# Kernel optimization log

Measured on AMD Instinct MI355X. Metric: run time of the kernel, lower is better.

## Reference

```python
import jax, jax.numpy as jnp
import numpy as np
from jax import lax

B, T, F = 8, 512, 128          # batch, mel time, mel freq
DM, DS, DC, EXP, NL = 384, 16, 4, 2, 12
DI = EXP * DM                   # 768 inner width
DTR = (DM + 15) // 16           # 24, mamba_ssm dt_rank='auto'
PT = PF = 16
L = (T // PT) * (F // PF)       # 256 patches
NC = 4


def setup_inputs() -> dict:
    key = jax.random.key(0)
    ks = iter(jax.random.split(key, 24))
    def n(shape, s=0.02):
        return jax.random.normal(next(ks), shape, jnp.float32) * s
    return {
        "x": jax.random.normal(next(ks), (B, T, F), jnp.float32),
        "patch_w": n((DM, PT, PF)),
        "patch_b": jnp.zeros((DM,), jnp.float32),
        "pos_embed": n((1, L, DM)),
        "ln_g": jnp.ones((NL, DM), jnp.float32),
        "ln_b": jnp.zeros((NL, DM), jnp.float32),
        "in_proj_w": n((NL, 2 * DI, DM)),
        "conv_w": n((NL, DI, DC), 0.1),
        "conv_b": jnp.zeros((NL, DI), jnp.float32),
        "x_proj_w": n((NL, DTR + 2 * DS, DI)),
        "dt_proj_w": n((NL, DI, DTR), 0.1),
        "dt_proj_b": n((NL, DI), 0.1),
        "A_log": jnp.tile(jnp.log(jnp.arange(1, DS + 1, dtype=jnp.float32))[None, None, :], (NL, DI, 1)),
        "Dskip": jnp.ones((NL, DI), jnp.float32),
        "out_proj_w": n((NL, DM, DI)),
        "fn_g": jnp.ones((DM,), jnp.float32),
        "fn_b": jnp.zeros((DM,), jnp.float32),
        "head_w": n((NC, DM)),
        "head_b": jnp.zeros((NC,), jnp.float32),
    }


def _layernorm(x, g, b):
    m = x.mean(-1, keepdims=True)
    v = jnp.var(x, axis=-1, keepdims=True)
    return (x - m) * lax.rsqrt(v + 1e-5) * g + b


def _silu(v):
    return v * jax.nn.sigmoid(v)


def _mamba_block(x, p):
    # x: [B, L, DM]; residual Mamba block (pre-LN, dropout=identity in eval)
    ln_g, ln_b, Wi, cw, cb, Wx, Wdt, bdt, A_log, Dsk, Wo = p
    res = x
    h = _layernorm(x, ln_g, ln_b)
    xz = jnp.einsum('bld,ed->ble', h, Wi)          # [B,L,2*DI]
    u, z = jnp.split(xz, 2, axis=-1)
    # causal depthwise conv1d, kernel DC (small, unrolled)
    up = jnp.pad(u, ((0, 0), (DC - 1, 0), (0, 0)))
    u = sum(up[:, k:k + L, :] * cw[:, k] for k in range(DC)) + cb
    u = _silu(u)
    proj = jnp.einsum('bld,ed->ble', u, Wx)        # [B,L,DTR+2*DS]
    dt, Bm, Cm = jnp.split(proj, [DTR, DTR + DS], axis=-1)
    delta = jax.nn.softplus(jnp.einsum('blr,dr->bld', dt, Wdt) + bdt)  # [B,L,DI]
    A = -jnp.exp(A_log)                            # [DI, DS]
    dA = jnp.exp(delta[..., None] * A)             # [B,L,DI,DS]
    dBu = (delta * u)[..., None] * Bm[:, :, None, :]

    def step(hst, inp):
        dA_t, dBu_t, C_t = inp
        hst = dA_t * hst + dBu_t                   # [B,DI,DS]
        return hst, jnp.einsum('bdn,bn->bd', hst, C_t)

    h0 = jnp.zeros((x.shape[0], DI, DS), x.dtype)
    _, ys = lax.scan(step, h0, (dA.swapaxes(0, 1), dBu.swapaxes(0, 1), Cm.swapaxes(0, 1)))
    y = ys.swapaxes(0, 1) + u * Dsk                # [B,L,DI]
    y = y * _silu(z)
    return res + jnp.einsum('bld,ed->ble', y, Wo)


def reference(x, patch_w, patch_b, pos_embed, ln_g, ln_b, in_proj_w, conv_w, conv_b,
              x_proj_w, dt_proj_w, dt_proj_b, A_log, Dskip, out_proj_w,
              fn_g, fn_b, head_w, head_b):
    Bn = x.shape[0]
    # patch embed = non-overlapping 16x16 conv == blocked reshape + einsum
    patches = x.reshape(Bn, T // PT, PT, F // PF, PF)
    tok = jnp.einsum('bhpwq,dpq->bhwd', patches, patch_w) + patch_b
    tok = tok.reshape(Bn, L, DM) + pos_embed

    def layer(carry, p):
        return _mamba_block(carry, p), None

    tok, _ = lax.scan(layer, tok, (ln_g, ln_b, in_proj_w, conv_w, conv_b,
                                   x_proj_w, dt_proj_w, dt_proj_b, A_log, Dskip, out_proj_w))
    tok = _layernorm(tok, fn_g, fn_b)
    pooled = tok.mean(axis=1)
    return pooled @ head_w.T + head_b
```

## Files before the change

### kernel.cpp

```cpp
#include <hip/hip_runtime.h>
#include <math.h>

namespace {

constexpr int kB   = 8;
constexpr int kL   = 256;
constexpr int kTok = 2048;
constexpr int kDM  = 384;
constexpr int kDI  = 768;
constexpr int kDS  = 16;
constexpr int kDTR = 24;
constexpr int kPROJ = 56;
constexpr int kNL  = 12;

constexpr int kWIN  = 2 * kDI * kDM;
constexpr int kWOUT = kDM * kDI;
constexpr int kWX   = kPROJ * kDI;
constexpr int kWTOT = kWIN + kWOUT + kWX;

typedef float f32x4 __attribute__((ext_vector_type(4)));
typedef short short8 __attribute__((ext_vector_type(8)));

__device__ __forceinline__ float softplus_f(float x) {
  return (x > 20.f) ? x : log1pf(__expf(x));
}
__device__ __forceinline__ float silu_f(float x) {
  return x / (1.f + __expf(-x));
}
__device__ __forceinline__ unsigned short f2bf(float f) {
  union { float f; unsigned u; } v; v.f = f;
  unsigned r = v.u + 0x7FFFu + ((v.u >> 16) & 1u);
  return (unsigned short)(r >> 16);
}
__device__ __forceinline__ float bf2f(unsigned short u) {
  return __uint_as_float((unsigned)u << 16);
}

__global__ __launch_bounds__(256) void patch_gemm_k(
    const float* __restrict__ x, const float* __restrict__ Bw,
    const float* __restrict__ bias, const float* __restrict__ pos,
    float* __restrict__ C) {
  __shared__ float As[16][68];
  __shared__ float Bs[16][68];
  int tid = threadIdx.x;
  int bm = blockIdx.y * 64;
  int bn = blockIdx.x * 64;
  int lr = tid >> 2;
  int lk = (tid & 3) << 2;
  int tm = (tid >> 4) << 2;
  int tn = (tid & 15) << 2;
  float acc[4][4] = {};
  for (int k0 = 0; k0 < 256; k0 += 16) {
    {
      int token = bm + lr;
      int b = token >> 8, l = token & 255;
      int h = l >> 3, w = l & 7;
      int p = k0 >> 4;
      const float* ap = x + ((size_t)(b * 512) + h * 16 + p) * 128 + w * 16 + lk;
      float4 av = *(const float4*)ap;
      As[lk + 0][lr] = av.x; As[lk + 1][lr] = av.y;
      As[lk + 2][lr] = av.z; As[lk + 3][lr] = av.w;
    }
    {
      const float* bp = Bw + (size_t)(bn + lr) * 256 + k0 + lk;
      float4 bv = *(const float4*)bp;
      Bs[lk + 0][lr] = bv.x; Bs[lk + 1][lr] = bv.y;
      Bs[lk + 2][lr] = bv.z; Bs[lk + 3][lr] = bv.w;
    }
    __syncthreads();
    #pragma unroll
    for (int k = 0; k < 16; ++k) {
      float4 a = *(const float4*)&As[k][tm];
      float4 b = *(const float4*)&Bs[k][tn];
      float av[4] = {a.x, a.y, a.z, a.w};
      float bv[4] = {b.x, b.y, b.z, b.w};
      #pragma unroll
      for (int i = 0; i < 4; ++i)
        #pragma unroll
        for (int j = 0; j < 4; ++j)
          acc[i][j] = fmaf(av[i], bv[j], acc[i][j]);
    }
    __syncthreads();
  }
  #pragma unroll
  for (int i = 0; i < 4; ++i) {
    int row = bm + tm + i;
    #pragma unroll
    for (int j = 0; j < 4; ++j) {
      int col = bn + tn + j;
      C[(size_t)row * kDM + col] =
          acc[i][j] + bias[col] + pos[(size_t)(row & 255) * kDM + col];
    }
  }
}

__global__ __launch_bounds__(384) void lnpool_k(
    const float* __restrict__ in, float* __restrict__ pooled,
    const float* __restrict__ g, const float* __restrict__ bb) {
  int t = blockIdx.x, d = threadIdx.x;
  float v = in[(size_t)t * kDM + d];
  float s = v, s2 = v * v;
  #pragma unroll
  for (int m = 32; m >= 1; m >>= 1) {
    s  += __shfl_xor(s, m);
    s2 += __shfl_xor(s2, m);
  }
  __shared__ float ps[6], ps2[6];
  if ((d & 63) == 0) { ps[d >> 6] = s; ps2[d >> 6] = s2; }
  __syncthreads();
  float S = 0.f, S2 = 0.f;
  #pragma unroll
  for (int i = 0; i < 6; ++i) { S += ps[i]; S2 += ps2[i]; }
  float mean = S * (1.f / 384.f);
  float var  = S2 * (1.f / 384.f) - mean * mean;
  float r = rsqrtf(var + 1e-5f);
  float o = (v - mean) * r * g[d] + bb[d];
  atomicAdd(&pooled[(size_t)(t >> 8) * kDM + d], o * (1.f / 256.f));
}

__global__ __launch_bounds__(256) void convert_all_k(
    const float* __restrict__ w_in, const float* __restrict__ w_out,
    const float* __restrict__ w_x, unsigned short* __restrict__ dst,
    float* __restrict__ pooled_zero) {
  int layer = blockIdx.y;
  int tid = threadIdx.x;
  if (layer == 0 && blockIdx.x == 0) {
    for (int i = tid; i < kB * kDM; i += 256) pooled_zero[i] = 0.f;
  }
  int i4 = (blockIdx.x * 256 + tid) * 4;
  if (i4 >= kWTOT) return;
  const float* src;
  int off;
  if (i4 < kWIN) { src = w_in + (size_t)layer * kWIN; off = i4; }
  else if (i4 < kWIN + kWOUT) { src = w_out + (size_t)layer * kWOUT; off = i4 - kWIN; }
  else { src = w_x + (size_t)layer * kWX; off = i4 - kWIN - kWOUT; }
  float4 v = *(const float4*)(src + off);
  unsigned short o[4] = {f2bf(v.x), f2bf(v.y), f2bf(v.z), f2bf(v.w)};
  *(uint2*)(dst + (size_t)layer * kWTOT + i4) = *(const uint2*)o;
}

__global__ __launch_bounds__(256) void inproj_ln_k(
    const float* __restrict__ tok, const unsigned short* __restrict__ Bw,
    const float* __restrict__ g, const float* __restrict__ bb,
    unsigned short* __restrict__ Cbf, float* __restrict__ proj_zero) {
  __shared__ __align__(16) unsigned short As[4][64][8];
  __shared__ __align__(16) unsigned short Bs[4][128][8];
  __shared__ float smean[64], srstd[64];
  __shared__ float sg_[kDM], sb_[kDM];
  int tid = threadIdx.x;
  int bm = blockIdx.y * 64;
  int bn = blockIdx.x * 128;
  {
    int bid = blockIdx.y * 12 + blockIdx.x;
    for (int i = bid * 256 + tid; i < kTok * kPROJ; i += 384 * 256)
      proj_zero[i] = 0.f;
  }
  for (int i = tid; i < kDM; i += 256) { sg_[i] = g[i]; sb_[i] = bb[i]; }
  {
    int r = tid >> 2, quarter = tid & 3;
    const float* rp = tok + (size_t)(bm + r) * kDM + quarter * 96;
    float s = 0.f, s2 = 0.f;
    #pragma unroll
    for (int q = 0; q < 24; ++q) {
      float4 v = ((const float4*)rp)[q];
      s  += v.x + v.y + v.z + v.w;
      s2 += v.x * v.x + v.y * v.y + v.z * v.z + v.w * v.w;
    }
    s  += __shfl_xor(s, 1);  s2 += __shfl_xor(s2, 1);
    s  += __shfl_xor(s, 2);  s2 += __shfl_xor(s2, 2);
    if (quarter == 0) {
      float mean = s * (1.f / 384.f);
      float var  = s2 * (1.f / 384.f) - mean * mean;
      smean[r] = mean;
      srstd[r] = rsqrtf(var + 1e-5f);
    }
  }
  __syncthreads();
  int wave = tid >> 6, lane = tid & 63;
  int lm = lane & 15, lq = lane >> 4;
  int wm = (wave & 1) * 32, wn = (wave >> 1) * 64;
  f32x4 acc[2][4] = {};
  for (int k0 = 0; k0 < kDM; k0 += 32) {
    int ar = tid & 63, aq = tid >> 6;
    unsigned short av[8];
    {
      float mean = smean[ar], rstd = srstd[ar];
      const float* ap = tok + (size_t)(bm + ar) * kDM + k0 + aq * 8;
      float4 v0 = ((const float4*)ap)[0];
      float4 v1 = ((const float4*)ap)[1];
      float vv[8] = {v0.x, v0.y, v0.z, v0.w, v1.x, v1.y, v1.z, v1.w};
      #pragma unroll
      for (int j = 0; j < 8; ++j) {
        int k = k0 + aq * 8 + j;
        av[j] = f2bf((vv[j] - mean) * rstd * sg_[k] + sb_[k]);
      }
    }
    int br = tid & 127, bq0 = tid >> 7, bq1 = bq0 + 2;
    uint4 b0 = *(const uint4*)(Bw + (size_t)(bn + br) * kDM + k0 + bq0 * 8);
    uint4 b1 = *(const uint4*)(Bw + (size_t)(bn + br) * kDM + k0 + bq1 * 8);
    __syncthreads();
    *(uint4*)&As[aq][ar][0]  = *(const uint4*)av;
    *(uint4*)&Bs[bq0][br][0] = b0;
    *(uint4*)&Bs[bq1][br][0] = b1;
    __syncthreads();
    short8 bfrag[4];
    #pragma unroll
    for (int ni = 0; ni < 4; ++ni)
      bfrag[ni] = *(const short8*)&Bs[lq][wn + ni * 16 + lm][0];
    #pragma unroll
    for (int mi = 0; mi < 2; ++mi) {
      short8 afrag = *(const short8*)&As[lq][wm + mi * 16 + lm][0];
      #pragma unroll
      for (int ni = 0; ni < 4; ++ni)
        acc[mi][ni] = __builtin_amdgcn_mfma_f32_16x16x32_bf16(
            afrag, bfrag[ni], acc[mi][ni], 0, 0, 0);
    }
  }
  #pragma unroll
  for (int mi = 0; mi < 2; ++mi) {
    #pragma unroll
    for (int ni = 0; ni < 4; ++ni) {
      int grow0 = bm + wm + mi * 16 + lq * 4;
      int gcol = bn + wn + ni * 16 + lm;
      #pragma unroll
      for (int r = 0; r < 4; ++r)
        Cbf[(size_t)(grow0 + r) * (2 * kDI) + gcol] = f2bf(acc[mi][ni][r]);
    }
  }
}

__global__ __launch_bounds__(256) void xproj_conv_k(
    const unsigned short* __restrict__ xz, const unsigned short* __restrict__ Bw,
    const float* __restrict__ cw, const float* __restrict__ cb,
    float* __restrict__ proj, unsigned short* __restrict__ uT_bf,
    unsigned short* __restrict__ sgT_bf) {
  __shared__ __align__(16) unsigned short As[4][64][8];
  __shared__ __align__(16) unsigned short Bs[4][64][8];
  __shared__ float scw[128][4];
  __shared__ float scb[128];
  int tid = threadIdx.x;
  int bm = blockIdx.x * 64;
  int kbase = blockIdx.y * 128;
  int wave = tid >> 6, lane = tid & 63;
  int lm = lane & 15, lq = lane >> 4;
  int wm = wave * 16;
  f32x4 acc[4] = {};

  if (tid < 128) {
    *(float4*)&scw[tid][0] = *(const float4*)(cw + (size_t)(kbase + tid) * 4);
    scb[tid] = cb[kbase + tid];
  }
  __syncthreads();

  int ar = tid & 63;
  int aq = tid >> 6;
  int t = bm + ar;
  int b = t >> 8, l = t & 255;

  for (int kt = 0; kt < 4; ++kt) {
    int k0 = kbase + kt * 32;
    int dloc = kt * 32 + aq * 8;
    int dg = kbase + dloc;
    unsigned short av[8];
    {
      float vals[4][8];
      #pragma unroll
      for (int q = 0; q < 4; ++q) {
        if (l - 3 + q >= 0) {
          uint4 r = *(const uint4*)(xz + (size_t)(t - 3 + q) * (2 * kDI) + dg);
          const unsigned short* rs = (const unsigned short*)&r;
          #pragma unroll
          for (int j = 0; j < 8; ++j) vals[q][j] = bf2f(rs[j]);
        } else {
          #pragma unroll
          for (int j = 0; j < 8; ++j) vals[q][j] = 0.f;
        }
      }
      uint4 zr = *(const uint4*)(xz + (size_t)t * (2 * kDI) + kDI + dg);
      const unsigned short* zs = (const unsigned short*)&zr;
      #pragma unroll
      for (int j = 0; j < 8; ++j) {
        float a = scb[dloc + j];
        a = fmaf(vals[0][j], scw[dloc + j][0], a);
        a = fmaf(vals[1][j], scw[dloc + j][1], a);
        a = fmaf(vals[2][j], scw[dloc + j][2], a);
        a = fmaf(vals[3][j], scw[dloc + j][3], a);
        unsigned short ub = f2bf(silu_f(a));
        av[j] = ub;
        size_t rbase = ((size_t)b * kDI + dg + j) * kL + l;
        uT_bf[rbase] = ub;
        sgT_bf[rbase] = f2bf(silu_f(bf2f(zs[j])));
      }
    }
    int br = tid & 63, bq = tid >> 6;
    uint4 b0;
    if (br < kPROJ)
      b0 = *(const uint4*)(Bw + (size_t)br * kDI + k0 + bq * 8);
    else
      b0 = make_uint4(0u, 0u, 0u, 0u);
    __syncthreads();
    *(uint4*)&As[aq][ar][0] = *(const uint4*)av;
    *(uint4*)&Bs[bq][br][0] = b0;
    __syncthreads();
    short8 afrag = *(const short8*)&As[lq][wm + lm][0];
    #pragma unroll
    for (int ni = 0; ni < 4; ++ni) {
      short8 bfrag = *(const short8*)&Bs[lq][ni * 16 + lm][0];
      acc[ni] = __builtin_amdgcn_mfma_f32_16x16x32_bf16(
          afrag, bfrag, acc[ni], 0, 0, 0);
    }
  }

  #pragma unroll
  for (int ni = 0; ni < 4; ++ni) {
    int grow0 = bm + wm + lq * 4;
    int gcol = ni * 16 + lm;
    if (gcol < kPROJ) {
      #pragma unroll
      for (int r = 0; r < 4; ++r)
        atomicAdd(&proj[(size_t)(grow0 + r) * kPROJ + gcol], acc[ni][r]);
    }
  }
}

__global__ __launch_bounds__(256) void bgemm_out_k(
    const unsigned short* __restrict__ A, int lda,
    const unsigned short* __restrict__ B, int ldb,
    float* __restrict__ C, int ldc, int Kc) {
  __shared__ __align__(16) unsigned short As[4][128][8];
  __shared__ __align__(16) unsigned short Bs[4][128][8];
  int tid = threadIdx.x;
  int bm = blockIdx.y * 128;
  int bn = blockIdx.x * 128;
  int k_begin = blockIdx.z * Kc;
  int wave = tid >> 6, lane = tid & 63;
  int lm = lane & 15, lq = lane >> 4;
  int wm = (wave >> 1) * 64, wn = (wave & 1) * 64;
  f32x4 acc[4][4] = {};

  for (int kt = 0; kt < Kc; kt += 32) {
    int k0 = k_begin + kt;
    int ar0 = tid & 127, aq0 = tid >> 7;
    int aq1 = aq0 + 2;
    uint4 a0 = *(const uint4*)(A + (size_t)(bm + ar0) * lda + k0 + aq0 * 8);
    uint4 a1 = *(const uint4*)(A + (size_t)(bm + ar0) * lda + k0 + aq1 * 8);
    uint4 b0 = *(const uint4*)(B + (size_t)(bn + ar0) * ldb + k0 + aq0 * 8);
    uint4 b1 = *(const uint4*)(B + (size_t)(bn + ar0) * ldb + k0 + aq1 * 8);
    __syncthreads();
    *(uint4*)&As[aq0][ar0][0] = a0;
    *(uint4*)&As[aq1][ar0][0] = a1;
    *(uint4*)&Bs[aq0][ar0][0] = b0;
    *(uint4*)&Bs[aq1][ar0][0] = b1;
    __syncthreads();
    short8 bfrag[4];
    #pragma unroll
    for (int ni = 0; ni < 4; ++ni)
      bfrag[ni] = *(const short8*)&Bs[lq][wn + ni * 16 + lm][0];
    #pragma unroll
    for (int mi = 0; mi < 4; ++mi) {
      short8 afrag = *(const short8*)&As[lq][wm + mi * 16 + lm][0];
      #pragma unroll
      for (int ni = 0; ni < 4; ++ni)
        acc[mi][ni] = __builtin_amdgcn_mfma_f32_16x16x32_bf16(
            afrag, bfrag[ni], acc[mi][ni], 0, 0, 0);
    }
  }

  #pragma unroll
  for (int mi = 0; mi < 4; ++mi) {
    #pragma unroll
    for (int ni = 0; ni < 4; ++ni) {
      int grow0 = bm + wm + mi * 16 + lq * 4;
      int gcol = bn + wn + ni * 16 + lm;
      #pragma unroll
      for (int r = 0; r < 4; ++r)
        atomicAdd(&C[(size_t)(grow0 + r) * ldc + gcol], acc[mi][ni][r]);
    }
  }
}

__global__ __launch_bounds__(256) void scansplit_k(
    const float* __restrict__ proj, const unsigned short* __restrict__ uT_bf,
    const unsigned short* __restrict__ sgT_bf, const float* __restrict__ dtw,
    const float* __restrict__ dtb, const float* __restrict__ A_log,
    const float* __restrict__ Dsk, unsigned short* __restrict__ y_bf) {
  int d0 = blockIdx.x * 8;
  int b = blockIdx.y;
  int tid = threadIdx.x;
  int dsub = tid & 7;
  int nh = (tid >> 3) & 1;
  int c = tid >> 4;
  int d = d0 + dsub;
  __shared__ float sh[16][16][9];
  __shared__ float sca[16][16][9];

  float Av[8];
  {
    const float* ap = A_log + (size_t)d * kDS + nh * 8;
    #pragma unroll
    for (int q = 0; q < 2; ++q) {
      float4 v = ((const float4*)ap)[q];
      Av[q * 4 + 0] = -__expf(v.x);
      Av[q * 4 + 1] = -__expf(v.y);
      Av[q * 4 + 2] = -__expf(v.z);
      Av[q * 4 + 3] = -__expf(v.w);
    }
  }
  float bdt = dtb[d];
  float Dv = Dsk[d];

  const float* pr = proj + ((size_t)(b * kL) + c * 16) * kPROJ;

  float dtlo[8], dthi[8];
  {
    float wdt[24];
    const float* wp = dtw + (size_t)d * kDTR;
    #pragma unroll
    for (int q = 0; q < 6; ++q) {
      float4 v = ((const float4*)wp)[q];
      wdt[q * 4 + 0] = v.x; wdt[q * 4 + 1] = v.y;
      wdt[q * 4 + 2] = v.z; wdt[q * 4 + 3] = v.w;
    }
    const float* prm = pr + (size_t)(nh * 8) * kPROJ;
    float mine[8];
    #pragma unroll
    for (int i = 0; i < 8; ++i) {
      const float* p = prm + (size_t)i * kPROJ;
      float acc = bdt;
      #pragma unroll
      for (int q = 0; q < 6; ++q) {
        float4 v = ((const float4*)p)[q];
        acc = fmaf(v.x, wdt[q * 4 + 0], acc);
        acc = fmaf(v.y, wdt[q * 4 + 1], acc);
        acc = fmaf(v.z, wdt[q * 4 + 2], acc);
        acc = fmaf(v.w, wdt[q * 4 + 3], acc);
      }
      mine[i] = softplus_f(acc);
    }
    #pragma unroll
    for (int i = 0; i < 8; ++i) {
      float other = __shfl_xor(mine[i], 8);
      dtlo[i] = nh ? other : mine[i];
      dthi[i] = nh ? mine[i] : other;
    }
  }

  float u_[16];
  {
    const unsigned short* up = uT_bf + ((size_t)b * kDI + d) * kL + c * 16;
    uint4 v0 = ((const uint4*)up)[0];
    uint4 v1 = ((const uint4*)up)[1];
    const unsigned short* us = (const unsigned short*)&v0;
    #pragma unroll
    for (int i = 0; i < 8; ++i) u_[i] = bf2f(us[i]);
    us = (const unsigned short*)&v1;
    #pragma unroll
    for (int i = 0; i < 8; ++i) u_[8 + i] = bf2f(us[i]);
  }

  float h[8], ca[8];
  #pragma unroll
  for (int n = 0; n < 8; ++n) { h[n] = 0.f; ca[n] = 1.f; }
  #pragma unroll
  for (int i = 0; i < 16; ++i) {
    float dl = (i < 8) ? dtlo[i] : dthi[i - 8];
    float du = dl * u_[i];
    const float* p = pr + (size_t)i * kPROJ + 24 + nh * 8;
    float4 b0 = ((const float4*)p)[0];
    float4 b1 = ((const float4*)p)[1];
    float Bv[8] = {b0.x, b0.y, b0.z, b0.w, b1.x, b1.y, b1.z, b1.w};
    #pragma unroll
    for (int n = 0; n < 8; ++n) {
      float a = __expf(dl * Av[n]);
      h[n] = fmaf(a, h[n], du * Bv[n]);
      ca[n] *= a;
    }
  }
  {
    int nrow = nh * 8;
    #pragma unroll
    for (int q = 0; q < 8; ++q) {
      sh[c][nrow + q][dsub] = h[q];
      sca[c][nrow + q][dsub] = ca[q];
    }
  }
  __syncthreads();

  float h0[8];
  #pragma unroll
  for (int n = 0; n < 8; ++n) h0[n] = 0.f;
  {
    int nrow = nh * 8;
    for (int j = 0; j < c; ++j) {
      #pragma unroll
      for (int q = 0; q < 8; ++q)
        h0[q] = fmaf(sca[j][nrow + q][dsub], h0[q], sh[j][nrow + q][dsub]);
    }
  }

  float sg_[16];
  if (nh == 0) {
    const unsigned short* sp = sgT_bf + ((size_t)b * kDI + d) * kL + c * 16;
    uint4 v0 = ((const uint4*)sp)[0];
    uint4 v1 = ((const uint4*)sp)[1];
    const unsigned short* ss = (const unsigned short*)&v0;
    #pragma unroll
    for (int i = 0; i < 8; ++i) sg_[i] = bf2f(ss[i]);
    ss = (const unsigned short*)&v1;
    #pragma unroll
    for (int i = 0; i < 8; ++i) sg_[8 + i] = bf2f(ss[i]);
  }

  unsigned short* yp = y_bf + (size_t)(b * kL + c * 16) * kDI + d;
  #pragma unroll
  for (int i = 0; i < 16; ++i) {
    float dl = (i < 8) ? dtlo[i] : dthi[i - 8];
    float du = dl * u_[i];
    const float* p = pr + (size_t)i * kPROJ + 24 + nh * 8;
    float4 b0 = ((const float4*)p)[0];
    float4 b1 = ((const float4*)p)[1];
    float4 c0 = ((const float4*)(p + 16))[0];
    float4 c1 = ((const float4*)(p + 16))[1];
    float Bv[8] = {b0.x, b0.y, b0.z, b0.w, b1.x, b1.y, b1.z, b1.w};
    float Cv[8] = {c0.x, c0.y, c0.z, c0.w, c1.x, c1.y, c1.z, c1.w};
    float yv = 0.f;
    #pragma unroll
    for (int n = 0; n < 8; ++n) {
      float a = __expf(dl * Av[n]);
      h0[n] = fmaf(a, h0[n], du * Bv[n]);
      yv = fmaf(h0[n], Cv[n], yv);
    }
    yv += __shfl_xor(yv, 8);
    if (nh == 0) yp[(size_t)i * kDI] = f2bf((yv + u_[i] * Dv) * sg_[i]);
  }
}

__global__ __launch_bounds__(64) void head_k(
    const float* __restrict__ pooled, const float* __restrict__ hw,
    const float* __restrict__ hb, float* __restrict__ out) {
  int b = blockIdx.x >> 2, c = blockIdx.x & 3;
  int lane = threadIdx.x;
  float acc = 0.f;
  for (int dd = lane; dd < kDM; dd += 64)
    acc = fmaf(pooled[b * kDM + dd], hw[c * kDM + dd], acc);
  #pragma unroll
  for (int m = 32; m >= 1; m >>= 1) acc += __shfl_xor(acc, m);
  if (lane == 0) out[b * 4 + c] = acc + hb[c];
}

}

extern "C" void kernel_launch(void* const* d_in, const int* in_sizes, int n_in,
                              void* d_out, int out_size, void* d_ws, size_t ws_size,
                              hipStream_t stream) {
  (void)in_sizes; (void)n_in; (void)out_size; (void)ws_size;
  const float* x        = (const float*)d_in[0];
  const float* patch_w  = (const float*)d_in[1];
  const float* patch_b  = (const float*)d_in[2];
  const float* pos      = (const float*)d_in[3];
  const float* ln_g     = (const float*)d_in[4];
  const float* ln_b     = (const float*)d_in[5];
  const float* in_w     = (const float*)d_in[6];
  const float* conv_w   = (const float*)d_in[7];
  const float* conv_b   = (const float*)d_in[8];
  const float* xproj_w  = (const float*)d_in[9];
  const float* dtproj_w = (const float*)d_in[10];
  const float* dtproj_b = (const float*)d_in[11];
  const float* A_log    = (const float*)d_in[12];
  const float* Dskip    = (const float*)d_in[13];
  const float* out_w    = (const float*)d_in[14];
  const float* fn_g     = (const float*)d_in[15];
  const float* fn_b     = (const float*)d_in[16];
  const float* head_w   = (const float*)d_in[17];
  const float* head_b   = (const float*)d_in[18];
  float* out = (float*)d_out;

  float* ws = (float*)d_ws;
  float* tok    = ws; ws += kTok * kDM;
  float* proj   = ws; ws += kTok * kPROJ;
  float* pooled = ws; ws += kB * kDM;
  unsigned short* xz_bf  = (unsigned short*)ws; ws += kTok * 2 * kDI / 2;
  unsigned short* uT_bf  = (unsigned short*)ws; ws += kTok * kDI / 2;
  unsigned short* sgT_bf = (unsigned short*)ws; ws += kTok * kDI / 2;
  unsigned short* y_bf   = (unsigned short*)ws; ws += kTok * kDI / 2;
  unsigned short* w_bf   = (unsigned short*)ws; ws += (size_t)kNL * kWTOT / 2;

  convert_all_k<<<dim3(kWTOT / 4 / 256, kNL), 256, 0, stream>>>(
      in_w, out_w, xproj_w, w_bf, pooled);

  patch_gemm_k<<<dim3(6, 32), 256, 0, stream>>>(x, patch_w, patch_b, pos, tok);

  for (int layer = 0; layer < kNL; ++layer) {
    const unsigned short* wl = w_bf + (size_t)layer * kWTOT;
    inproj_ln_k<<<dim3(12, 32), 256, 0, stream>>>(
        tok, wl, ln_g + layer * kDM, ln_b + layer * kDM, xz_bf, proj);
    xproj_conv_k<<<dim3(32, 6), 256, 0, stream>>>(
        xz_bf, wl + kWIN + kWOUT, conv_w + layer * kDI * 4,
        conv_b + layer * kDI, proj, uT_bf, sgT_bf);
    scansplit_k<<<dim3(kDI / 8, kB), 256, 0, stream>>>(
        proj, uT_bf, sgT_bf, dtproj_w + (size_t)layer * kDI * kDTR,
        dtproj_b + layer * kDI, A_log + (size_t)layer * kDI * kDS,
        Dskip + layer * kDI, y_bf);
    bgemm_out_k<<<dim3(3, 16, 4), 256, 0, stream>>>(
        y_bf, kDI, wl + kWIN, kDI, tok, kDM, kDI / 4);
  }

  lnpool_k<<<kTok, kDM, 0, stream>>>(tok, pooled, fn_g, fn_b);
  head_k<<<kB * 4, 64, 0, stream>>>(pooled, head_w, head_b, out);
}
```

Measured before the change: 1.146 ms.

## Fuse in-projection, causal conv and x-projection into one kernel per layer

Merges the LayerNorm+in_proj GEMM with the depthwise causal conv, SiLU and x_proj GEMM into a single kernel. Each block handles 32 tokens plus a 3-token halo and one 128-channel slice of u and its matching z slice, so the bf16 xz intermediate never goes to global memory and one launch per layer is removed. The proj zeroing moves into patch_gemm and the out-projection kernel so the following layer's atomics start from zero. The cost is recomputing the halo rows (35 of every 48 MMA rows are useful), more shared memory per block, and a grid of 384 blocks.

```diff
diff --git a/kernel.cpp b/kernel.cpp
--- a/kernel.cpp
+++ b/kernel.cpp
@@ -39,12 +39,17 @@
 __global__ __launch_bounds__(256) void patch_gemm_k(
     const float* __restrict__ x, const float* __restrict__ Bw,
     const float* __restrict__ bias, const float* __restrict__ pos,
-    float* __restrict__ C) {
+    float* __restrict__ C, float* __restrict__ proj_zero) {
   __shared__ float As[16][68];
   __shared__ float Bs[16][68];
   int tid = threadIdx.x;
   int bm = blockIdx.y * 64;
   int bn = blockIdx.x * 64;
+  {
+    int bid = blockIdx.y * 6 + blockIdx.x;
+    for (int i = bid * 256 + tid; i < kTok * kPROJ; i += 192 * 256)
+      proj_zero[i] = 0.f;
+  }
   int lr = tid >> 2;
   int lk = (tid & 3) << 2;
   int tm = (tid >> 4) << 2;
@@ -139,26 +144,39 @@
   *(uint2*)(dst + (size_t)layer * kWTOT + i4) = *(const uint2*)o;
 }
 
-__global__ __launch_bounds__(256) void inproj_ln_k(
-    const float* __restrict__ tok, const unsigned short* __restrict__ Bw,
-    const float* __restrict__ g, const float* __restrict__ bb,
-    unsigned short* __restrict__ Cbf, float* __restrict__ proj_zero) {
-  __shared__ __align__(16) unsigned short As[4][64][8];
-  __shared__ __align__(16) unsigned short Bs[4][128][8];
-  __shared__ float smean[64], srstd[64];
+__global__ __launch_bounds__(256) void fused1_k(
+    const float* __restrict__ tok, const unsigned short* __restrict__ Win,
+    const unsigned short* __restrict__ Wx, const float* __restrict__ g,
+    const float* __restrict__ bb, const float* __restrict__ cw,
+    const float* __restrict__ cb, float* __restrict__ proj,
+    unsigned short* __restrict__ uT_bf, unsigned short* __restrict__ sgT_bf) {
+  __shared__ float smean[35], srstd[35];
   __shared__ float sg_[kDM], sb_[kDM];
+  __shared__ __align__(16) unsigned short As[4][48][8];
+  __shared__ __align__(16) unsigned short Bs[4][256][8];
+  __shared__ float scw[128][4];
+  __shared__ float scb[128];
+  __shared__ __align__(16) unsigned short upre[35][128];
+  __shared__ __align__(16) unsigned short xa[32][128];
+  __shared__ __align__(16) unsigned short Bs2[64][128];
+
   int tid = threadIdx.x;
-  int bm = blockIdx.y * 64;
-  int bn = blockIdx.x * 128;
-  {
-    int bid = blockIdx.y * 12 + blockIdx.x;
-    for (int i = bid * 256 + tid; i < kTok * kPROJ; i += 384 * 256)
-      proj_zero[i] = 0.f;
-  }
+  int bm = blockIdx.x * 32;
+  int kb = blockIdx.y * 128;
+  int wave = tid >> 6, lane = tid & 63;
+  int lm = lane & 15, lq = lane >> 4;
+  int l0 = bm & 255;
+
   for (int i = tid; i < kDM; i += 256) { sg_[i] = g[i]; sb_[i] = bb[i]; }
-  {
+  if (tid < 128) {
+    *(float4*)&scw[tid][0] = *(const float4*)(cw + (size_t)(kb + tid) * 4);
+    scb[tid] = cb[kb + tid];
+  }
+  if (tid < 140) {
     int r = tid >> 2, quarter = tid & 3;
-    const float* rp = tok + (size_t)(bm + r) * kDM + quarter * 96;
+    int t = bm + r - 3;
+    int tc = t < 0 ? 0 : t;
+    const float* rp = tok + (size_t)tc * kDM + quarter * 96;
     float s = 0.f, s2 = 0.f;
     #pragma unroll
     for (int q = 0; q < 24; ++q) {
@@ -176,149 +194,138 @@
     }
   }
   __syncthreads();
-  int wave = tid >> 6, lane = tid & 63;
-  int lm = lane & 15, lq = lane >> 4;
-  int wm = (wave & 1) * 32, wn = (wave >> 1) * 64;
-  f32x4 acc[2][4] = {};
+
+  int ar = tid >> 2, aq = tid & 3;
+  int wn = wave * 64;
+  f32x4 acc[3][4] = {};
   for (int k0 = 0; k0 < kDM; k0 += 32) {
-    int ar = tid & 63, aq = tid >> 6;
     unsigned short av[8];
-    {
-      float mean = smean[ar], rstd = srstd[ar];
-      const float* ap = tok + (size_t)(bm + ar) * kDM + k0 + aq * 8;
+    if (ar < 48) {
+      int t = bm + ar - 3;
+      bool zr = (ar < 3) && (l0 == 0);
+      int tc = t < 0 ? 0 : (t > kTok - 1 ? kTok - 1 : t);
+      int sidx = ar < 35 ? ar : 34;
+      float mean = smean[sidx], rstd = srstd[sidx];
+      const float* ap = tok + (size_t)tc * kDM + k0 + aq * 8;
       float4 v0 = ((const float4*)ap)[0];
       float4 v1 = ((const float4*)ap)[1];
       float vv[8] = {v0.x, v0.y, v0.z, v0.w, v1.x, v1.y, v1.z, v1.w};
       #pragma unroll
       for (int j = 0; j < 8; ++j) {
         int k = k0 + aq * 8 + j;
-        av[j] = f2bf((vv[j] - mean) * rstd * sg_[k] + sb_[k]);
+        float val = zr ? 0.f : (vv[j] - mean) * rstd * sg_[k] + sb_[k];
+        av[j] = f2bf(val);
       }
     }
-    int br = tid & 127, bq0 = tid >> 7, bq1 = bq0 + 2;
-    uint4 b0 = *(const uint4*)(Bw + (size_t)(bn + br) * kDM + k0 + bq0 * 8);
-    uint4 b1 = *(const uint4*)(Bw + (size_t)(bn + br) * kDM + k0 + bq1 * 8);
+    uint4 bv[4];
+    {
+      int br = tid;
+      size_t wrow = (br < 128) ? (size_t)(kb + br) : (size_t)(kDI + kb + br - 128);
+      const unsigned short* wp = Win + wrow * kDM + k0;
+      #pragma unroll
+      for (int q = 0; q < 4; ++q) bv[q] = *(const uint4*)(wp + q * 8);
+    }
     __syncthreads();
-    *(uint4*)&As[aq][ar][0]  = *(const uint4*)av;
-    *(uint4*)&Bs[bq0][br][0] = b0;
-    *(uint4*)&Bs[bq1][br][0] = b1;
+    if (ar < 48) *(uint4*)&As[aq][ar][0] = *(const uint4*)av;
+    #pragma unroll
+    for (int q = 0; q < 4; ++q) *(uint4*)&Bs[q][tid][0] = bv[q];
     __syncthreads();
     short8 bfrag[4];
     #pragma unroll
     for (int ni = 0; ni < 4; ++ni)
       bfrag[ni] = *(const short8*)&Bs[lq][wn + ni * 16 + lm][0];
     #pragma unroll
-    for (int mi = 0; mi < 2; ++mi) {
-      short8 afrag = *(const short8*)&As[lq][wm + mi * 16 + lm][0];
+    for (int mi = 0; mi < 3; ++mi) {
+      short8 afrag = *(const short8*)&As[lq][mi * 16 + lm][0];
       #pragma unroll
       for (int ni = 0; ni < 4; ++ni)
         acc[mi][ni] = __builtin_amdgcn_mfma_f32_16x16x32_bf16(
             afrag, bfrag[ni], acc[mi][ni], 0, 0, 0);
     }
   }
-  #pragma unroll
-  for (int mi = 0; mi < 2; ++mi) {
+  __syncthreads();
+
+  #pragma unroll
+  for (int mi = 0; mi < 3; ++mi) {
     #pragma unroll
     for (int ni = 0; ni < 4; ++ni) {
-      int grow0 = bm + wm + mi * 16 + lq * 4;
-      int gcol = bn + wn + ni * 16 + lm;
-      #pragma unroll
-      for (int r = 0; r < 4; ++r)
-        Cbf[(size_t)(grow0 + r) * (2 * kDI) + gcol] = f2bf(acc[mi][ni][r]);
-    }
-  }
-}
-
-__global__ __launch_bounds__(256) void xproj_conv_k(
-    const unsigned short* __restrict__ xz, const unsigned short* __restrict__ Bw,
-    const float* __restrict__ cw, const float* __restrict__ cb,
-    float* __restrict__ proj, unsigned short* __restrict__ uT_bf,
-    unsigned short* __restrict__ sgT_bf) {
-  __shared__ __align__(16) unsigned short As[4][64][8];
-  __shared__ __align__(16) unsigned short Bs[4][64][8];
-  __shared__ float scw[128][4];
-  __shared__ float scb[128];
-  int tid = threadIdx.x;
-  int bm = blockIdx.x * 64;
-  int kbase = blockIdx.y * 128;
-  int wave = tid >> 6, lane = tid & 63;
-  int lm = lane & 15, lq = lane >> 4;
-  int wm = wave * 16;
-  f32x4 acc[4] = {};
-
-  if (tid < 128) {
-    *(float4*)&scw[tid][0] = *(const float4*)(cw + (size_t)(kbase + tid) * 4);
-    scb[tid] = cb[kbase + tid];
-  }
-  __syncthreads();
-
-  int ar = tid & 63;
-  int aq = tid >> 6;
-  int t = bm + ar;
-  int b = t >> 8, l = t & 255;
-
-  for (int kt = 0; kt < 4; ++kt) {
-    int k0 = kbase + kt * 32;
-    int dloc = kt * 32 + aq * 8;
-    int dg = kbase + dloc;
-    unsigned short av[8];
-    {
-      float vals[4][8];
-      #pragma unroll
-      for (int q = 0; q < 4; ++q) {
-        if (l - 3 + q >= 0) {
-          uint4 r = *(const uint4*)(xz + (size_t)(t - 3 + q) * (2 * kDI) + dg);
-          const unsigned short* rs = (const unsigned short*)&r;
-          #pragma unroll
-          for (int j = 0; j < 8; ++j) vals[q][j] = bf2f(rs[j]);
-        } else {
-          #pragma unroll
-          for (int j = 0; j < 8; ++j) vals[q][j] = 0.f;
+      int col = wn + ni * 16 + lm;
+      #pragma unroll
+      for (int r = 0; r < 4; ++r) {
+        int row = mi * 16 + lq * 4 + r;
+        if (row < 35) {
+          float v = acc[mi][ni][r];
+          if (col < 128) {
+            upre[row][col] = f2bf(v);
+          } else if (row >= 3) {
+            int t = bm + row - 3;
+            sgT_bf[((size_t)(t >> 8) * kDI + kb + col - 128) * kL + (t & 255)] =
+                f2bf(silu_f(v));
+          }
         }
       }
-      uint4 zr = *(const uint4*)(xz + (size_t)t * (2 * kDI) + kDI + dg);
-      const unsigned short* zs = (const unsigned short*)&zr;
-      #pragma unroll
-      for (int j = 0; j < 8; ++j) {
-        float a = scb[dloc + j];
-        a = fmaf(vals[0][j], scw[dloc + j][0], a);
-        a = fmaf(vals[1][j], scw[dloc + j][1], a);
-        a = fmaf(vals[2][j], scw[dloc + j][2], a);
-        a = fmaf(vals[3][j], scw[dloc + j][3], a);
-        unsigned short ub = f2bf(silu_f(a));
-        av[j] = ub;
-        size_t rbase = ((size_t)b * kDI + dg + j) * kL + l;
-        uT_bf[rbase] = ub;
-        sgT_bf[rbase] = f2bf(silu_f(bf2f(zs[j])));
+    }
+  }
+  for (int idx = tid; idx < 64 * 16; idx += 256) {
+    int row = idx >> 4, q = idx & 15;
+    uint4 v;
+    if (row < kPROJ)
+      v = *(const uint4*)(Wx + (size_t)row * kDI + kb + q * 8);
+    else
+      v = make_uint4(0u, 0u, 0u, 0u);
+    *(uint4*)&Bs2[row][q * 8] = v;
+  }
+  __syncthreads();
+
+  {
+    int dloc = tid & 127;
+    int lh = tid >> 7;
+    float w0 = scw[dloc][0], w1 = scw[dloc][1];
+    float w2 = scw[dloc][2], w3 = scw[dloc][3];
+    float cbv = scb[dloc];
+    #pragma unroll
+    for (int i = 0; i < 16; ++i) {
+      int l = lh * 16 + i;
+      float a = cbv;
+      a = fmaf(bf2f(upre[l + 0][dloc]), w0, a);
+      a = fmaf(bf2f(upre[l + 1][dloc]), w1, a);
+      a = fmaf(bf2f(upre[l + 2][dloc]), w2, a);
+      a = fmaf(bf2f(upre[l + 3][dloc]), w3, a);
+      float uval = silu_f(a);
+      unsigned short ub = f2bf(uval);
+      xa[l][dloc] = ub;
+      int t = bm + l;
+      uT_bf[((size_t)(t >> 8) * kDI + kb + dloc) * kL + (t & 255)] = ub;
+    }
+  }
+  __syncthreads();
+
+  {
+    int kq = wave;
+    f32x4 acc2[2][4] = {};
+    #pragma unroll
+    for (int mi = 0; mi < 2; ++mi) {
+      short8 afrag = *(const short8*)&xa[mi * 16 + lm][kq * 32 + lq * 8];
+      #pragma unroll
+      for (int ni = 0; ni < 4; ++ni) {
+        short8 bfrag = *(const short8*)&Bs2[ni * 16 + lm][kq * 32 + lq * 8];
+        acc2[mi][ni] = __builtin_amdgcn_mfma_f32_16x16x32_bf16(
+            afrag, bfrag, acc2[mi][ni], 0, 0, 0);
       }
     }
-    int br = tid & 63, bq = tid >> 6;
-    uint4 b0;
-    if (br < kPROJ)
-      b0 = *(const uint4*)(Bw + (size_t)br * kDI + k0 + bq * 8);
-    else
-      b0 = make_uint4(0u, 0u, 0u, 0u);
-    __syncthreads();
-    *(uint4*)&As[aq][ar][0] = *(const uint4*)av;
-    *(uint4*)&Bs[bq][br][0] = b0;
-    __syncthreads();
-    short8 afrag = *(const short8*)&As[lq][wm + lm][0];
-    #pragma unroll
-    for (int ni = 0; ni < 4; ++ni) {
-      short8 bfrag = *(const short8*)&Bs[lq][ni * 16 + lm][0];
-      acc[ni] = __builtin_amdgcn_mfma_f32_16x16x32_bf16(
-          afrag, bfrag, acc[ni], 0, 0, 0);
-    }
-  }
-
-  #pragma unroll
-  for (int ni = 0; ni < 4; ++ni) {
-    int grow0 = bm + wm + lq * 4;
-    int gcol = ni * 16 + lm;
-    if (gcol < kPROJ) {
-      #pragma unroll
-      for (int r = 0; r < 4; ++r)
-        atomicAdd(&proj[(size_t)(grow0 + r) * kPROJ + gcol], acc[ni][r]);
+    #pragma unroll
+    for (int mi = 0; mi < 2; ++mi) {
+      #pragma unroll
+      for (int ni = 0; ni < 4; ++ni) {
+        int col = ni * 16 + lm;
+        if (col < kPROJ) {
+          #pragma unroll
+          for (int r = 0; r < 4; ++r) {
+            int trow = bm + mi * 16 + lq * 4 + r;
+            atomicAdd(&proj[(size_t)trow * kPROJ + col], acc2[mi][ni][r]);
+          }
+        }
+      }
     }
   }
 }
@@ -326,13 +333,18 @@
 __global__ __launch_bounds__(256) void bgemm_out_k(
     const unsigned short* __restrict__ A, int lda,
     const unsigned short* __restrict__ B, int ldb,
-    float* __restrict__ C, int ldc, int Kc) {
+    float* __restrict__ C, int ldc, int Kc, float* __restrict__ proj_zero) {
   __shared__ __align__(16) unsigned short As[4][128][8];
   __shared__ __align__(16) unsigned short Bs[4][128][8];
   int tid = threadIdx.x;
   int bm = blockIdx.y * 128;
   int bn = blockIdx.x * 128;
   int k_begin = blockIdx.z * Kc;
+  {
+    int bid = (blockIdx.z * 16 + blockIdx.y) * 3 + blockIdx.x;
+    for (int i = bid * 256 + tid; i < kTok * kPROJ; i += 192 * 256)
+      proj_zero[i] = 0.f;
+  }
   int wave = tid >> 6, lane = tid & 63;
   int lm = lane & 15, lq = lane >> 4;
   int wm = (wave >> 1) * 64, wn = (wave & 1) * 64;
@@ -579,7 +591,6 @@
   float* tok    = ws; ws += kTok * kDM;
   float* proj   = ws; ws += kTok * kPROJ;
   float* pooled = ws; ws += kB * kDM;
-  unsigned short* xz_bf  = (unsigned short*)ws; ws += kTok * 2 * kDI / 2;
   unsigned short* uT_bf  = (unsigned short*)ws; ws += kTok * kDI / 2;
   unsigned short* sgT_bf = (unsigned short*)ws; ws += kTok * kDI / 2;
   unsigned short* y_bf   = (unsigned short*)ws; ws += kTok * kDI / 2;
@@ -588,21 +599,20 @@
   convert_all_k<<<dim3(kWTOT / 4 / 256, kNL), 256, 0, stream>>>(
       in_w, out_w, xproj_w, w_bf, pooled);
 
-  patch_gemm_k<<<dim3(6, 32), 256, 0, stream>>>(x, patch_w, patch_b, pos, tok);
+  patch_gemm_k<<<dim3(6, 32), 256, 0, stream>>>(x, patch_w, patch_b, pos, tok,
+                                                proj);
 
   for (int layer = 0; layer < kNL; ++layer) {
     const unsigned short* wl = w_bf + (size_t)layer * kWTOT;
-    inproj_ln_k<<<dim3(12, 32), 256, 0, stream>>>(
-        tok, wl, ln_g + layer * kDM, ln_b + layer * kDM, xz_bf, proj);
-    xproj_conv_k<<<dim3(32, 6), 256, 0, stream>>>(
-        xz_bf, wl + kWIN + kWOUT, conv_w + layer * kDI * 4,
-        conv_b + layer * kDI, proj, uT_bf, sgT_bf);
+    fused1_k<<<dim3(64, 6), 256, 0, stream>>>(
+        tok, wl, wl + kWIN + kWOUT, ln_g + layer * kDM, ln_b + layer * kDM,
+        conv_w + layer * kDI * 4, conv_b + layer * kDI, proj, uT_bf, sgT_bf);
     scansplit_k<<<dim3(kDI / 8, kB), 256, 0, stream>>>(
         proj, uT_bf, sgT_bf, dtproj_w + (size_t)layer * kDI * kDTR,
         dtproj_b + layer * kDI, A_log + (size_t)layer * kDI * kDS,
         Dskip + layer * kDI, y_bf);
     bgemm_out_k<<<dim3(3, 16, 4), 256, 0, stream>>>(
-        y_bf, kDI, wl + kWIN, kDI, tok, kDM, kDI / 4);
+        y_bf, kDI, wl + kWIN, kDI, tok, kDM, kDI / 4, proj);
   }
 
   lnpool_k<<<kTok, kDM, 0, stream>>>(tok, pooled, fn_g, fn_b);
```

After: 1.482 ms. +29.3%, slower.
